# Optimization experiments

Hardware: AMD Instinct MI355X
Metric: run time of the kernel (lower is better)

## Reference

```python
import jax, jax.numpy as jnp
import numpy as np

PAD = float(-2**32 + 1)
NUM_HEADS = 16
LN_EPS = 1e-5


def _split_heads(x, h):
    # torch.cat(torch.chunk(x, h, dim=2), dim=0): head-major stacking
    B, T, D = x.shape
    d = D // h
    return x.reshape(B, T, h, d).transpose(2, 0, 1, 3).reshape(h * B, T, d)


def _merge_heads(x, h):
    # torch.cat(torch.chunk(x, h, dim=0), dim=2)
    hB, T, d = x.shape
    B = hB // h
    return x.reshape(h, B, T, d).transpose(1, 2, 0, 3).reshape(B, T, h * d)


def setup_inputs() -> dict:
    key = jax.random.key(0)
    ks = jax.random.split(key, 12)
    B, T, D = 2, 2048, 1024
    s = 1.0 / np.sqrt(D)
    return {
        "q": jax.random.normal(ks[0], (B, T, D), jnp.float32),
        "k": jax.random.normal(ks[1], (B, T, D), jnp.float32),
        "v": jax.random.normal(ks[2], (B, T, D), jnp.float32),
        "mask": jax.random.randint(ks[3], (B, T), 0, 2, jnp.int32),
        "causality": 0,
        "edge_fea": jnp.zeros((1,), jnp.float32),
        "wq": jax.random.normal(ks[4], (D, D), jnp.float32) * s,
        "bq": jax.random.normal(ks[5], (D,), jnp.float32) * 0.01,
        "wk": jax.random.normal(ks[6], (D, D), jnp.float32) * s,
        "bk": jax.random.normal(ks[7], (D,), jnp.float32) * 0.01,
        "wv": jax.random.normal(ks[8], (D, D), jnp.float32) * s,
        "bv": jax.random.normal(ks[9], (D,), jnp.float32) * 0.01,
        "gamma": jnp.ones((D,), jnp.float32),
        "beta": jnp.zeros((D,), jnp.float32),
    }


def reference(q, k, v, mask, causality, edge_fea, wq, bq, wk, bk, wv, bv, gamma, beta):
    h = NUM_HEADS
    B, T, D = q.shape
    depth = D // h

    qh = _split_heads(q @ wq.T + bq, h)   # (h*B, T, depth)
    kh = _split_heads(k @ wk.T + bk, h)
    vh = _split_heads(v @ wv.T + bv, h)

    scores = jnp.einsum('ntd,nsd->nts', qh, kh) / jnp.sqrt(jnp.asarray(depth, qh.dtype))
    # key mask: repeat_interleave over dim 0 (batch-major), 1 => masked
    km = jnp.repeat(mask.astype(scores.dtype), h, axis=0)[:, None, :]  # (h*B,1,T)
    scores = scores + km * PAD
    if causality:
        tril = jnp.tril(jnp.ones((T, T), scores.dtype))
        scores = jnp.where(tril[None] == 0, jnp.full_like(scores, PAD), scores)
    attn = jax.nn.softmax(scores, axis=-1)
    ctx = jnp.einsum('nts,nsd->ntd', attn, vh)

    out = _merge_heads(ctx, h) + q  # dropout is identity in eval mode
    # LayerNorm over last dim
    mu = jnp.mean(out, axis=-1, keepdims=True)
    var = jnp.var(out, axis=-1, keepdims=True)
    out = (out - mu) / jnp.sqrt(var + LN_EPS) * gamma + beta
    return out
```

## Files before the change

### kernel.cpp

```cpp
#include <hip/hip_runtime.h>
#include <hip/hip_bf16.h>
#include <stdint.h>

#define B_ 2
#define T_ 2048
#define D_ 1024
#define H_ 16
#define DEPTH 64

typedef unsigned short u16;
typedef unsigned int u32;
typedef short bf16x8 __attribute__((ext_vector_type(8)));
typedef float f32x4 __attribute__((ext_vector_type(4)));
typedef float f32x16 __attribute__((ext_vector_type(16)));

#define MFMA16(a, b, c) __builtin_amdgcn_mfma_f32_16x16x32_bf16(a, b, c, 0, 0, 0)
#define MFMA32(a, b, c) __builtin_amdgcn_mfma_f32_32x32x16_bf16(a, b, c, 0, 0, 0)

#if __has_builtin(__builtin_amdgcn_exp2f)
#define EXP2(x) __builtin_amdgcn_exp2f(x)
#else
#define EXP2(x) __expf((x) * 0.6931471805599453f)
#endif

#define GLOAD_LDS(g, l)                                                      \
    __builtin_amdgcn_global_load_lds(                                        \
        (__attribute__((address_space(1))) void*)(g),                        \
        (__attribute__((address_space(3))) void*)(l), 16, 0, 0)

__device__ __forceinline__ float bf2f(u32 u) {
    union { u32 i; float f; } x; x.i = u << 16; return x.f;
}
__device__ __forceinline__ u16 f2bf(float f) {
    union { float f; u32 i; } x; x.f = f;
    u32 r = x.i + 0x7fffu + ((x.i >> 16) & 1u);
    return (u16)(r >> 16);
}
__device__ __forceinline__ uint2 pk4(float4 f) {
    return make_uint2((u32)f2bf(f.x) | ((u32)f2bf(f.y) << 16),
                      (u32)f2bf(f.z) | ((u32)f2bf(f.w) << 16));
}
__device__ __forceinline__ u32 cvtpk(float lo, float hi) {
    u32 r;
    asm("v_cvt_pk_bf16_f32 %0, %1, %2" : "=v"(r) : "v"(lo), "v"(hi));
    return r;
}
__device__ __forceinline__ bf16x8 pk_frag(u32 a, u32 b, u32 c, u32 d) {
    union { u32 u[4]; bf16x8 v; } x;
    x.u[0] = a; x.u[1] = b; x.u[2] = c; x.u[3] = d;
    return x.v;
}
__device__ __forceinline__ f32x16 zero16() {
    f32x16 z;
    #pragma unroll
    for (int i = 0; i < 16; ++i) z[i] = 0.f;
    return z;
}

__global__ __launch_bounds__(256) void convw_kernel(
    const float* __restrict__ s0, const float* __restrict__ s1, const float* __restrict__ s2,
    u16* __restrict__ wbf)
{
    const int z = blockIdx.y;
    const float* src = (z == 0) ? s0 : (z == 1) ? s1 : s2;
    u16* dst = wbf + (size_t)z * 1048576;
    for (size_t i = ((size_t)blockIdx.x * 256 + threadIdx.x) * 8; i < 1048576u;
         i += (size_t)gridDim.x * 2048) {
        float4 a = *(const float4*)(src + i);
        float4 b = *(const float4*)(src + i + 4);
        uint2 lo = pk4(a), hi = pk4(b);
        *(uint4*)(dst + i) = make_uint4(lo.x, lo.y, hi.x, hi.y);
    }
}

__global__ __launch_bounds__(256, 3) void proj_mfma(
    const float* __restrict__ qf, const float* __restrict__ kf, const float* __restrict__ vf,
    const u16* __restrict__ wbf,
    const float* __restrict__ bq, const float* __restrict__ bk, const float* __restrict__ bv,
    u16* __restrict__ qh, u16* __restrict__ kh, u16* __restrict__ vt)
{
    __shared__ __attribute__((aligned(16))) u16 SH[128 * 132];
    u16* As = SH;
    u16* Bs = SH + 8192;

    const int lin = blockIdx.x + 8 * blockIdx.y + 256 * blockIdx.z;
    const int swz = (lin & 7) * 96 + (lin >> 3);
    const int bx = swz & 7;
    const int by = (swz >> 3) & 31;
    const int z  = swz >> 8;

    const float* X = (z == 0) ? qf : (z == 1) ? kf : vf;
    const u16* W = wbf + (size_t)z * 1048576;
    const float* bias = (z == 0) ? bq : (z == 1) ? bk : bv;

    const int tid = threadIdx.x, w = tid >> 6, lane = tid & 63;
    const int quad = lane >> 4, l16 = lane & 15;
    const int m0 = by * 128, n0 = bx * 128;
    const int wm = (w & 1) * 64, wn = (w >> 1) * 64;
    const int srow = lane >> 3;
    const int schunk = (lane & 7) ^ srow;

    const int xr = tid >> 3;
    const int xc = tid & 7;
    const int xsw = (xc ^ (xr & 7)) * 8;

    f32x4 acc[4][4];
    #pragma unroll
    for (int mi = 0; mi < 4; ++mi)
        #pragma unroll
        for (int ni = 0; ni < 4; ++ni) acc[mi][ni] = (f32x4){0.f, 0.f, 0.f, 0.f};

    const size_t br = (size_t)(n0 + 32 * w + srow);

    for (int k0 = 0; k0 < D_; k0 += 64) {
        __syncthreads();
        #pragma unroll
        for (int i = 0; i < 4; ++i)
            GLOAD_LDS(W + (br + 8 * i) * D_ + k0 + schunk * 8, &Bs[(32 * w + 8 * i) * 64]);
        #pragma unroll
        for (int u = 0; u < 4; ++u) {
            const int row = u * 32 + xr;
            const float* p = X + (size_t)(m0 + row) * D_ + k0 + xc * 8;
            float4 a0 = *(const float4*)p;
            float4 a1 = *(const float4*)(p + 4);
            uint4 pv;
            pv.x = cvtpk(a0.x, a0.y); pv.y = cvtpk(a0.z, a0.w);
            pv.z = cvtpk(a1.x, a1.y); pv.w = cvtpk(a1.z, a1.w);
            *(uint4*)&As[row * 64 + xsw] = pv;
        }
        __syncthreads();

        #pragma unroll
        for (int kg = 0; kg < 2; ++kg) {
            const int ch = ((4 * kg + quad) ^ (l16 & 7)) * 8;
            bf16x8 af[4], bf[4];
            #pragma unroll
            for (int mi = 0; mi < 4; ++mi)
                af[mi] = *(const bf16x8*)&As[(wm + 16 * mi + l16) * 64 + ch];
            #pragma unroll
            for (int ni = 0; ni < 4; ++ni)
                bf[ni] = *(const bf16x8*)&Bs[(wn + 16 * ni + l16) * 64 + ch];
            #pragma unroll
            for (int mi = 0; mi < 4; ++mi)
                #pragma unroll
                for (int ni = 0; ni < 4; ++ni)
                    acc[mi][ni] = MFMA16(af[mi], bf[ni], acc[mi][ni]);
        }
    }

    float bl[4];
    #pragma unroll
    for (int ni = 0; ni < 4; ++ni) bl[ni] = bias[n0 + wn + ni * 16 + l16];

    __syncthreads();

    if (z < 2) {
        #pragma unroll
        for (int mi = 0; mi < 4; ++mi) {
            #pragma unroll
            for (int ni = 0; ni < 4; ++ni) {
                const int nn = wn + ni * 16 + l16;
                #pragma unroll
                for (int r = 0; r < 4; ++r) {
                    const int tl = wm + mi * 16 + quad * 4 + r;
                    SH[tl * 132 + nn] = f2bf(acc[mi][ni][r] + bl[ni]);
                }
            }
        }
    } else {
        #pragma unroll
        for (int mi = 0; mi < 4; ++mi) {
            const int t4 = wm + mi * 16 + quad * 4;
            const int tp4 = (t4 & ~12) | ((t4 & 4) << 1) | ((t4 & 8) >> 1);
            #pragma unroll
            for (int ni = 0; ni < 4; ++ni) {
                const int nn = wn + ni * 16 + l16;
                float4 f = make_float4(acc[mi][ni][0] + bl[ni], acc[mi][ni][1] + bl[ni],
                                       acc[mi][ni][2] + bl[ni], acc[mi][ni][3] + bl[ni]);
                *(uint2*)&SH[nn * 132 + tp4] = pk4(f);
            }
        }
    }
    __syncthreads();

    {
        const int ch = tid & 31;
        const int r0 = tid >> 5;
        const int b  = m0 >> 11;
        const int tb = m0 & (T_ - 1);
        if (z < 2) {
            u16* outp = (z == 0) ? qh : kh;
            const int hd = ch >> 4;
            const int head = (n0 >> 6) + hd;
            const int dd = (ch & 15) * 4;
            #pragma unroll
            for (int s = 0; s < 16; ++s) {
                const int tl = r0 + s * 8;
                uint2 vv = *(const uint2*)&SH[tl * 132 + hd * 64 + dd];
                *(uint2*)(outp + ((size_t)(head * B_ + b) * T_ + tb + tl) * DEPTH + dd) = vv;
            }
        } else {
            #pragma unroll
            for (int s = 0; s < 16; ++s) {
                const int nn = r0 + s * 8;
                const int nng = n0 + nn;
                const int head = nng >> 6, d = nng & 63;
                uint2 vv = *(const uint2*)&SH[nn * 132 + ch * 4];
                *(uint2*)(vt + ((size_t)(head * B_ + b) * DEPTH + d) * T_ + tb + ch * 4) = vv;
            }
        }
    }
}

__global__ __launch_bounds__(256, 4) void attn_kernel(
    const u16* __restrict__ qh, const u16* __restrict__ kh, const u16* __restrict__ vt,
    const int* __restrict__ maskp, const int* __restrict__ causp,
    u16* __restrict__ po, float* __restrict__ pl)
{
    __shared__ __attribute__((aligned(16))) u16 Ks[2][64 * 64];
    __shared__ __attribute__((aligned(16))) u16 Vs[2][64 * 64];
    __shared__ __attribute__((aligned(16))) float padf[1024];

    const int lin = blockIdx.x + 16 * blockIdx.y + 512 * blockIdx.z;
    const int swz = (lin & 7) * 128 + (lin >> 3);
    const int qt = swz & 15;
    const int n  = (swz >> 4) & 31;
    const int kk = swz >> 9;

    const int kbase = kk * 1024;
    const int head = n >> 1, bi = n & 1;
    const int mrow = n >> 4;
    const int caus = causp[0];

    const int tid  = threadIdx.x;
    const int w    = tid >> 6, lane = tid & 63;
    const int l32  = lane & 31, h = lane >> 5;
    const size_t base  = (size_t)n * T_ * DEPTH;
    const size_t vbase = (size_t)n * DEPTH * T_;
    const size_t elems = (size_t)B_ * T_ * D_;

    const float C1  = 0.18033688011112042f;
    const float PL2 = -6.2e9f;

    {
        const int i0 = tid * 4;
        int4 m = *(const int4*)(maskp + (size_t)mrow * T_ + kbase + i0);
        padf[i0 + 0] = (float)m.x * PL2; padf[i0 + 1] = (float)m.y * PL2;
        padf[i0 + 2] = (float)m.z * PL2; padf[i0 + 3] = (float)m.w * PL2;
    }

    const int qg = qt * 128 + w * 32 + l32;
    bf16x8 aq[4];
    #pragma unroll
    for (int c = 0; c < 4; ++c)
        aq[c] = *(const bf16x8*)(qh + base + (size_t)qg * DEPTH + c * 16 + h * 8);

    f32x16 O0 = zero16(), O1 = zero16();
    float lp = 0.f;

    const int g_row = w * 16 + (lane >> 3);
    const int g_ch  = (lane & 7) ^ ((lane >> 3) & 7);
    const u16* ksrc = kh + base + (size_t)g_row * DEPTH + g_ch * 8;
    const u16* vsrc = vt + vbase + (size_t)g_row * T_ + g_ch * 8;

#define STAGE(bf_, t0_)                                                           \
    do {                                                                          \
        GLOAD_LDS(ksrc + (size_t)(t0_) * DEPTH,       &Ks[bf_][(w * 16) * 64]);   \
        GLOAD_LDS(ksrc + (size_t)((t0_) + 8) * DEPTH, &Ks[bf_][(w * 16 + 8) * 64]); \
        GLOAD_LDS(vsrc + (t0_),                       &Vs[bf_][(w * 16) * 64]);   \
        GLOAD_LDS(vsrc + (size_t)8 * T_ + (t0_),      &Vs[bf_][(w * 16 + 8) * 64]); \
    } while (0)

    STAGE(0, kbase);
    __syncthreads();

    for (int it = 0; it < 16; ++it) {
        const int cur = it & 1;
        if (it < 15) STAGE(cur ^ 1, kbase + (it + 1) * 64);

        const int lt0 = it * 64;
        bf16x8 pa[2][2];
        #pragma unroll
        for (int kb = 0; kb < 2; ++kb) {
            const int krow = kb * 32 + l32;
            const u16* krp = &Ks[cur][krow * 64];
            const int ksw = krow & 7;
            f32x16 st = zero16();
            #pragma unroll
            for (int c = 0; c < 4; ++c) {
                bf16x8 kf = *(const bf16x8*)(krp + (((c * 2 + h) ^ ksw) * 8));
                st = MFMA32(kf, aq[c], st);
            }
            u32 pk[8];
            #pragma unroll
            for (int g = 0; g < 4; ++g) {
                f32x4 pv = *(const f32x4*)&padf[lt0 + kb * 32 + g * 8 + h * 4];
                #pragma unroll
                for (int m2 = 0; m2 < 2; ++m2) {
                    const int r0 = g * 4 + m2 * 2;
                    float v0 = fmaf(st[r0],     C1, pv[m2 * 2]);
                    float v1 = fmaf(st[r0 + 1], C1, pv[m2 * 2 + 1]);
                    if (caus) {
                        const int kg = kbase + lt0 + kb * 32 + g * 8 + h * 4 + m2 * 2;
                        if (kg     > qg) v0 = PL2;
                        if (kg + 1 > qg) v1 = PL2;
                    }
                    const float e0 = EXP2(v0), e1 = EXP2(v1);
                    lp += e0 + e1;
                    pk[g * 2 + m2] = cvtpk(e0, e1);
                }
            }
            pa[kb][0] = pk_frag(pk[0], pk[1], pk[2], pk[3]);
            pa[kb][1] = pk_frag(pk[4], pk[5], pk[6], pk[7]);
        }

        #pragma unroll
        for (int dblk = 0; dblk < 2; ++dblk) {
            const int d = dblk * 32 + l32;
            const u16* vrp = &Vs[cur][d * 64];
            const int vsw = d & 7;
            #pragma unroll
            for (int kb = 0; kb < 2; ++kb)
                #pragma unroll
                for (int kc = 0; kc < 2; ++kc) {
                    const int ch = (kb * 4 + kc * 2 + h) ^ vsw;
                    bf16x8 vf = *(const bf16x8*)(vrp + ch * 8);
                    if (dblk == 0) O0 = MFMA32(pa[kb][kc], vf, O0);
                    else           O1 = MFMA32(pa[kb][kc], vf, O1);
                }
        }

        __syncthreads();
    }
#undef STAGE

    lp += __shfl_xor(lp, 32, 64);
    u16* pop = po + (size_t)kk * elems;
    float* plp = pl + (size_t)kk * 32 * T_;
    if (lane < 32)
        plp[(size_t)n * T_ + qt * 128 + w * 32 + l32] = lp;

    #pragma unroll
    for (int r = 0; r < 16; ++r) {
        const int q = qt * 128 + w * 32 + (r & 3) + 8 * (r >> 2) + 4 * h;
        const size_t rb = ((size_t)bi * T_ + q) * D_ + head * DEPTH + l32;
        pop[rb]      = f2bf(O0[r]);
        pop[rb + 32] = f2bf(O1[r]);
    }
}

__global__ __launch_bounds__(256) void fuse_ln(
    const u16* __restrict__ po, const float* __restrict__ pl,
    const float* __restrict__ qin,
    const float* __restrict__ gamma, const float* __restrict__ beta,
    float* __restrict__ out)
{
    const int row = blockIdx.x;
    const int bi = row >> 11, t = row & (T_ - 1);
    const int tid = threadIdx.x;
    const size_t elems = (size_t)B_ * T_ * D_;

    const int head = tid >> 4;
    const size_t li = (size_t)(head * B_ + bi) * T_ + t;
    const float l = pl[li] + pl[32 * T_ + li];
    const float inv = 1.0f / fmaxf(l, 1e-30f);

    const size_t basei = (size_t)row * D_ + (tid << 2);
    uint2 a = *(const uint2*)(po + basei);
    uint2 b = *(const uint2*)(po + elems + basei);
    float4 qv = *(const float4*)(qin + basei);
    float x[4];
    x[0] = (bf2f(a.x & 0xffffu) + bf2f(b.x & 0xffffu)) * inv + qv.x;
    x[1] = (bf2f(a.x >> 16)     + bf2f(b.x >> 16))     * inv + qv.y;
    x[2] = (bf2f(a.y & 0xffffu) + bf2f(b.y & 0xffffu)) * inv + qv.z;
    x[3] = (bf2f(a.y >> 16)     + bf2f(b.y >> 16))     * inv + qv.w;

    float s  = x[0] + x[1] + x[2] + x[3];
    float s2 = x[0]*x[0] + x[1]*x[1] + x[2]*x[2] + x[3]*x[3];
    #pragma unroll
    for (int off = 1; off < 64; off <<= 1) {
        s  += __shfl_xor(s, off, 64);
        s2 += __shfl_xor(s2, off, 64);
    }
    __shared__ float rs[4], rs2[4];
    const int wid = tid >> 6;
    if ((tid & 63) == 0) { rs[wid] = s; rs2[wid] = s2; }
    __syncthreads();
    s  = rs[0] + rs[1] + rs[2] + rs[3];
    s2 = rs2[0] + rs2[1] + rs2[2] + rs2[3];
    const float mean = s * (1.0f / (float)D_);
    const float var  = s2 * (1.0f / (float)D_) - mean * mean;
    const float rstd = rsqrtf(var + 1e-5f);
    float4 g = *(const float4*)(gamma + (tid << 2));
    float4 bb = *(const float4*)(beta + (tid << 2));
    float4 r;
    r.x = (x[0] - mean) * rstd * g.x + bb.x;
    r.y = (x[1] - mean) * rstd * g.y + bb.y;
    r.z = (x[2] - mean) * rstd * g.z + bb.z;
    r.w = (x[3] - mean) * rstd * g.w + bb.w;
    *(float4*)(out + basei) = r;
}

extern "C" void kernel_launch(void* const* d_in, const int* in_sizes, int n_in,
                              void* d_out, int out_size, void* d_ws, size_t ws_size,
                              hipStream_t stream)
{
    (void)in_sizes; (void)n_in; (void)out_size; (void)ws_size;
    const float* q    = (const float*)d_in[0];
    const float* k    = (const float*)d_in[1];
    const float* v    = (const float*)d_in[2];
    const int* mask = (const int*)d_in[3];
    const int* caus = (const int*)d_in[4];
    const float* wq = (const float*)d_in[6];
    const float* bq = (const float*)d_in[7];
    const float* wk = (const float*)d_in[8];
    const float* bk = (const float*)d_in[9];
    const float* wv = (const float*)d_in[10];
    const float* bv = (const float*)d_in[11];
    const float* gamma = (const float*)d_in[12];
    const float* beta  = (const float*)d_in[13];
    float* out = (float*)d_out;

    const size_t elems = (size_t)B_ * T_ * D_;
    u16* qh  = (u16*)d_ws;
    u16* kh  = qh + elems;
    u16* vt  = kh + elems;
    u16* wbf = vt + elems;
    u16* po  = wbf + 3 * 1048576;
    float* pl = (float*)(po + 2 * elems);

    convw_kernel<<<dim3(64, 3), 256, 0, stream>>>(wq, wk, wv, wbf);
    proj_mfma<<<dim3(8, 32, 3), 256, 0, stream>>>(q, k, v, wbf, bq, bk, bv, qh, kh, vt);

    dim3 agrid(T_ / 128, H_ * B_, 2);
    attn_kernel<<<agrid, 256, 0, stream>>>(qh, kh, vt, mask, caus, po, pl);

    fuse_ln<<<B_ * T_, 256, 0, stream>>>(po, pl, q, gamma, beta, out);
}
```

Baseline: 227.7 us.

## Double-buffer weight tiles in LDS and load activations directly into registers

The projection GEMM now double-buffers the bf16 weight tile in shared memory, prefetching the next k-slice while computing the current one, so there is one barrier per iteration instead of two. The fp32 activation tile no longer goes through LDS. Each wave reads its A fragments straight from global memory and converts them to bf16 in registers. This removes the LDS staging and a sync, but every wave sharing the same rows now issues redundant global reads of X, and those loads are not prefetched, so latency may be exposed.

```diff
diff --git a/kernel.cpp b/kernel.cpp
--- a/kernel.cpp
+++ b/kernel.cpp
@@ -80,8 +80,6 @@
     u16* __restrict__ qh, u16* __restrict__ kh, u16* __restrict__ vt)
 {
     __shared__ __attribute__((aligned(16))) u16 SH[128 * 132];
-    u16* As = SH;
-    u16* Bs = SH + 8192;
 
     const int lin = blockIdx.x + 8 * blockIdx.y + 256 * blockIdx.z;
     const int swz = (lin & 7) * 96 + (lin >> 3);
@@ -100,10 +98,6 @@
     const int srow = lane >> 3;
     const int schunk = (lane & 7) ^ srow;
 
-    const int xr = tid >> 3;
-    const int xc = tid & 7;
-    const int xsw = (xc ^ (xr & 7)) * 8;
-
     f32x4 acc[4][4];
     #pragma unroll
     for (int mi = 0; mi < 4; ++mi)
@@ -111,48 +105,54 @@
         for (int ni = 0; ni < 4; ++ni) acc[mi][ni] = (f32x4){0.f, 0.f, 0.f, 0.f};
 
     const size_t br = (size_t)(n0 + 32 * w + srow);
-
-    for (int k0 = 0; k0 < D_; k0 += 64) {
-        __syncthreads();
-        #pragma unroll
-        for (int i = 0; i < 4; ++i)
-            GLOAD_LDS(W + (br + 8 * i) * D_ + k0 + schunk * 8, &Bs[(32 * w + 8 * i) * 64]);
-        #pragma unroll
-        for (int u = 0; u < 4; ++u) {
-            const int row = u * 32 + xr;
-            const float* p = X + (size_t)(m0 + row) * D_ + k0 + xc * 8;
-            float4 a0 = *(const float4*)p;
-            float4 a1 = *(const float4*)(p + 4);
-            uint4 pv;
-            pv.x = cvtpk(a0.x, a0.y); pv.y = cvtpk(a0.z, a0.w);
-            pv.z = cvtpk(a1.x, a1.y); pv.w = cvtpk(a1.z, a1.w);
-            *(uint4*)&As[row * 64 + xsw] = pv;
-        }
-        __syncthreads();
+    const int ar = m0 + wm + l16;
+    const int ac = quad * 8;
+
+    #pragma unroll
+    for (int i = 0; i < 4; ++i)
+        GLOAD_LDS(W + (br + 8 * i) * D_ + schunk * 8, &SH[(32 * w + 8 * i) * 64]);
+    __syncthreads();
+
+    for (int it = 0; it < 16; ++it) {
+        const int cur = it & 1;
+        const int k0 = it * 64;
+        const u16* Bsc = SH + cur * 8192;
+        if (it < 15) {
+            u16* Bsn = (u16*)SH + (cur ^ 1) * 8192;
+            #pragma unroll
+            for (int i = 0; i < 4; ++i)
+                GLOAD_LDS(W + (br + 8 * i) * D_ + (k0 + 64) + schunk * 8,
+                          &Bsn[(32 * w + 8 * i) * 64]);
+        }
 
         #pragma unroll
         for (int kg = 0; kg < 2; ++kg) {
             const int ch = ((4 * kg + quad) ^ (l16 & 7)) * 8;
             bf16x8 af[4], bf[4];
             #pragma unroll
-            for (int mi = 0; mi < 4; ++mi)
-                af[mi] = *(const bf16x8*)&As[(wm + 16 * mi + l16) * 64 + ch];
+            for (int mi = 0; mi < 4; ++mi) {
+                const float* p = X + (size_t)(ar + 16 * mi) * D_ + k0 + kg * 32 + ac;
+                float4 a0 = *(const float4*)p;
+                float4 a1 = *(const float4*)(p + 4);
+                af[mi] = pk_frag(cvtpk(a0.x, a0.y), cvtpk(a0.z, a0.w),
+                                 cvtpk(a1.x, a1.y), cvtpk(a1.z, a1.w));
+            }
             #pragma unroll
             for (int ni = 0; ni < 4; ++ni)
-                bf[ni] = *(const bf16x8*)&Bs[(wn + 16 * ni + l16) * 64 + ch];
+                bf[ni] = *(const bf16x8*)&Bsc[(wn + 16 * ni + l16) * 64 + ch];
             #pragma unroll
             for (int mi = 0; mi < 4; ++mi)
                 #pragma unroll
                 for (int ni = 0; ni < 4; ++ni)
                     acc[mi][ni] = MFMA16(af[mi], bf[ni], acc[mi][ni]);
         }
+
+        __syncthreads();
     }
 
     float bl[4];
     #pragma unroll
     for (int ni = 0; ni < 4; ++ni) bl[ni] = bias[n0 + wn + ni * 16 + l16];
-
-    __syncthreads();
 
     if (z < 2) {
         #pragma unroll
```

After: 269.5 us. 18.4% more time.
